# Optimization experiments

Measured on AMD Instinct MI355X. Metric: run time of the kernel, lower is better.

Reference implementation:

```python
import jax
import jax.numpy as jnp
from jax import lax
import numpy as np

N_LAYER = 8
SCALE = 4
H_CH = 128
Z_CH = 64


def conv2d(x, w, b=None, stride=1, pad=0):
    # x: NCHW, w: OIHW
    out = lax.conv_general_dilated(
        x, w, (stride, stride), [(pad, pad), (pad, pad)],
        dimension_numbers=("NCHW", "OIHW", "NCHW"))
    if b is not None:
        out = out + b[None, :, None, None]
    return out


def conv_transpose2d(x, w, stride):
    # torch ConvTranspose2d semantics, weight shape (in, out, kH, kW), no bias
    return lax.conv_transpose(
        x, w, (stride, stride), "VALID",
        dimension_numbers=("NCHW", "IOHW", "NCHW"), transpose_kernel=True)


def lstm_cell(inp, hidden, cell, gw, gb, tw, tb):
    # inp = inp + transform(hidden); gates fused into one conv (order f,i,o,s)
    inp = inp + conv2d(hidden, tw, tb, pad=2)
    gates = conv2d(inp, gw, gb, pad=2)
    f, i, o, s = jnp.split(gates, 4, axis=1)
    cell = jax.nn.sigmoid(f) * cell + jax.nn.sigmoid(i) * jnp.tanh(s)
    hidden = jax.nn.sigmoid(o) * jnp.tanh(cell)
    return hidden, cell


def setup_inputs() -> dict:
    key = jax.random.key(0)
    ks = jax.random.split(key, 24)
    b, xc, H, W = 64, 3, 64, 64
    vd, rd = 7, 256
    hs, ws = H // SCALE, W // SCALE
    enc_in = vd + rd + xc + H_CH   # 394
    dec_in = vd + rd + Z_CH        # 327

    def w_init(k, shape):
        fan_in = int(np.prod(shape[1:]))
        return jax.random.normal(k, shape, jnp.float32) / np.sqrt(fan_in)

    inp = {
        "x": jax.random.normal(ks[0], (b, xc, H, W), jnp.float32),
        "v": jax.random.normal(ks[1], (b, vd), jnp.float32),
        "r": jax.random.normal(ks[2], (b, rd, hs, ws), jnp.float32),
        "eps": jax.random.normal(ks[3], (N_LAYER, b, Z_CH, hs, ws), jnp.float32),
        "read_w": w_init(ks[4], (xc, xc, SCALE, SCALE)),
        "write_w": w_init(ks[5], (H_CH, H_CH, SCALE, SCALE)),  # (in,out,kH,kW)
        "prior_w": w_init(ks[6], (2 * Z_CH, H_CH, 5, 5)),
        "prior_b": jnp.zeros((2 * Z_CH,), jnp.float32),
        "post_w": w_init(ks[7], (2 * Z_CH, H_CH, 5, 5)),
        "post_b": jnp.zeros((2 * Z_CH,), jnp.float32),
        "enc_gw": w_init(ks[8], (4 * H_CH, enc_in, 5, 5)),
        "enc_gb": jnp.zeros((4 * H_CH,), jnp.float32),
        "enc_tw": w_init(ks[9], (enc_in, H_CH, 5, 5)),
        "enc_tb": jnp.zeros((enc_in,), jnp.float32),
        "dec_gw": w_init(ks[10], (4 * H_CH, dec_in, 5, 5)),
        "dec_gb": jnp.zeros((4 * H_CH,), jnp.float32),
        "dec_tw": w_init(ks[11], (dec_in, H_CH, 5, 5)),
        "dec_tb": jnp.zeros((dec_in,), jnp.float32),
        "obs_w": w_init(ks[12], (xc, H_CH, 1, 1)),
        "obs_b": jnp.zeros((xc,), jnp.float32),
    }
    return inp


def reference(x, v, r, eps, read_w, write_w, prior_w, prior_b, post_w, post_b,
              enc_gw, enc_gb, enc_tw, enc_tb, dec_gw, dec_gb, dec_tw, dec_tb,
              obs_w, obs_b):
    b, _, H, W = x.shape
    hs, ws = H // SCALE, W // SCALE
    dt = x.dtype
    h_enc = jnp.zeros((b, H_CH, hs, ws), dt)
    c_enc = jnp.zeros((b, H_CH, hs, ws), dt)
    h_dec = jnp.zeros((b, H_CH, hs, ws), dt)
    c_dec = jnp.zeros((b, H_CH, hs, ws), dt)
    u = jnp.zeros((b, H_CH, H, W), dt)

    xr = conv2d(x, read_w, stride=SCALE)            # (b, xc, hs, ws)
    vb = jnp.broadcast_to(v[:, :, None, None], (b, v.shape[1], hs, ws))
    rb = r if r.shape[2] == hs else jnp.tile(r, (1, 1, hs, ws))

    kl_loss = jnp.zeros((), dt)
    for t in range(N_LAYER):
        p_mu, p_lv = jnp.split(conv2d(h_dec, prior_w, prior_b, pad=2), 2, axis=1)
        h_enc, c_enc = lstm_cell(
            jnp.concatenate([h_dec, xr, vb, rb], axis=1),
            h_enc, c_enc, enc_gw, enc_gb, enc_tw, enc_tb)
        q_mu, q_lv = jnp.split(conv2d(h_enc, post_w, post_b, pad=2), 2, axis=1)
        z = q_mu + jnp.exp(0.5 * q_lv) * eps[t]
        h_dec, c_dec = lstm_cell(
            jnp.concatenate([z, vb, rb], axis=1),
            h_dec, c_dec, dec_gw, dec_gb, dec_tw, dec_tb)
        u = u + conv_transpose2d(h_dec, write_w, SCALE)
        # KL(q||p) with var = exp(logvar); log(var1/var0) = p_lv - q_lv
        kl = 0.5 * (jnp.exp(q_lv - p_lv)
                    + (p_mu - q_mu) ** 2 * jnp.exp(-p_lv)
                    - 1.0 + (p_lv - q_lv))
        kl_loss = kl_loss + kl.sum(axis=(1, 2, 3)).mean()

    canvas = jax.nn.sigmoid(conv2d(u, obs_w, obs_b))
    return canvas, kl_loss
```

## Files before the change

### kernel.cpp

```cpp
#include <hip/hip_runtime.h>
#include <hip/hip_bf16.h>

using bf16 = __hip_bfloat16;
typedef __attribute__((ext_vector_type(8))) short short8;
typedef __attribute__((ext_vector_type(4))) float f32x4;
typedef __attribute__((ext_vector_type(8))) int i32x8;
typedef __attribute__((ext_vector_type(4))) int i32x4;
typedef __attribute__((ext_vector_type(2))) int i32x2;

#define DEVI __device__ __forceinline__

#define MTOT 16384
#define PADS 25600

DEVI float sigm_(float x){ return 1.f/(1.f+expf(-x)); }

DEVI float s2f(short v){
  unsigned u = ((unsigned)(unsigned short)v) << 16;
  return __builtin_bit_cast(float, u);
}

DEVI long pidx_(int m){
  int nb = m>>8, iy=(m>>4)&15, ix=m&15;
  return (long)(nb*20 + iy + 2)*20 + (ix + 2);
}

DEVI unsigned char f2fp8(float x){
  int p = __builtin_amdgcn_cvt_pk_fp8_f32(x, 0.f, 0, false);
  return (unsigned char)(p & 0xFF);
}
DEVI float fp82f(unsigned char v){
  return __builtin_amdgcn_cvt_f32_fp8((int)v, 0);
}

DEVI void async16(const void* g, void* l) {
  __builtin_amdgcn_global_load_lds(
      (__attribute__((address_space(1))) void*)(unsigned long long)g,
      (__attribute__((address_space(3))) void*)(unsigned int)(unsigned long long)l,
      16, 0, 0);
}

template<int N> DEVI void waitbar(){
  if constexpr (N==0)      asm volatile("s_waitcnt vmcnt(0)\ns_barrier" ::: "memory");
  else if constexpr (N==3) asm volatile("s_waitcnt vmcnt(3)\ns_barrier" ::: "memory");
  else                     asm volatile("s_waitcnt vmcnt(6)\ns_barrier" ::: "memory");
}

template<int CA, int NS>
DEVI void g8_core(const unsigned char* __restrict__ A8,
                  const unsigned char* __restrict__ Bt8,
                  int m0, int n0, unsigned char* AsB, unsigned char* BsB,
                  f32x4 (&acc)[4][4])
{
  constexpr int Kp8 = NS*128;
  const int tid = threadIdx.x;
  const int wv = tid>>6, ln = tid&63;

  const int rr = tid>>3;
  const int lc = (tid&7) ^ (rr&7);
  long paRC[4], pbR[4];
  #pragma unroll
  for (int i=0;i<4;i++){
    int m = m0 + rr + (i<<5);
    paRC[i] = (long)(((m>>8)*20 + ((m>>4)&15))*20 + (m&15)) * CA;
    pbR[i]  = (long)(n0 + rr + (i<<5))*Kp8 + lc*16;
  }

  int cc = lc*16, tp = 0, ks = 0;
  auto stage = [&](int d){
    const int shiftC = ((tp/5)*20 + (tp%5)) * CA;
    char* la = (char*)AsB + d*16384 + (wv<<10);
    char* lb = (char*)BsB + d*16384 + (wv<<10);
    #pragma unroll
    for (int i=0;i<4;i++) async16(A8 + paRC[i] + shiftC + cc, la + i*4096);
    #pragma unroll
    for (int i=0;i<4;i++) async16(Bt8 + pbR[i] + ks, lb + i*4096);
    cc += 128; if (cc >= CA){ cc -= CA; tp++; }
    ks += 128;
  };

  const int wm = wv>>1, wn = wv&1;
  const int rA0 = (wm<<6) + (ln&15);
  const int rB0 = (wn<<6) + (ln&15);
  const int xa = ln&7;
  const int q2 = (ln>>4)<<1;
  const int c0 = ((q2    ) ^ xa)<<4;
  const int c1 = ((q2 | 1) ^ xa)<<4;

  stage(0);
  for (int t=0; t<NS; ++t) {
    asm volatile("s_waitcnt vmcnt(0)\ns_barrier" ::: "memory");
    if (t+1 < NS) stage((t+1)&1);

    const char* as_ = (const char*)AsB + (t&1)*16384;
    const char* bs_ = (const char*)BsB + (t&1)*16384;
    i32x8 af[4], bfr[4];
    #pragma unroll
    for (int f=0; f<4; f++){
      const char* p = as_ + ((rA0 + (f<<4))<<7);
      ((i32x4*)&af[f])[0] = *(const i32x4*)(p + c0);
      ((i32x4*)&af[f])[1] = *(const i32x4*)(p + c1);
    }
    #pragma unroll
    for (int f=0; f<4; f++){
      const char* p = bs_ + ((rB0 + (f<<4))<<7);
      ((i32x4*)&bfr[f])[0] = *(const i32x4*)(p + c0);
      ((i32x4*)&bfr[f])[1] = *(const i32x4*)(p + c1);
    }
    __builtin_amdgcn_s_setprio(1);
    #pragma unroll
    for (int mf=0; mf<4; mf++)
      #pragma unroll
      for (int nf=0; nf<4; nf++)
        acc[mf][nf] = __builtin_amdgcn_mfma_scale_f32_16x16x128_f8f6f4(
            af[mf], bfr[nf], acc[mf][nf], 0, 0, 0, 127, 0, 122);
    __builtin_amdgcn_s_setprio(0);
  }
}

template<int CA, int NS>
__global__ __launch_bounds__(256)
void conv_g8(const unsigned char* __restrict__ A8,
             const unsigned char* __restrict__ Bt8,
             const float* __restrict__ bias, bf16* __restrict__ outB)
{
  __shared__ alignas(16) unsigned char As[2][16384];
  __shared__ alignas(16) unsigned char Bs[2][16384];
  const int m0 = blockIdx.x<<7, n0 = blockIdx.y<<7;
  f32x4 acc[4][4] = {};
  g8_core<CA,NS>(A8, Bt8, m0, n0, &As[0][0], &Bs[0][0], acc);

  const int tid = threadIdx.x;
  const int wv = tid>>6, ln = tid&63;
  const int mb = m0 + ((wv>>1)<<6);
  const int nb = n0 + ((wv&1)<<6);
  const int ml = (ln>>4)<<2;
  const int nl = ln&15;
  #pragma unroll
  for (int mf=0; mf<4; mf++)
    #pragma unroll
    for (int j=0; j<4; j++) {
      const int m = mb + (mf<<4) + ml + j;
      #pragma unroll
      for (int nf=0; nf<4; nf++) {
        const int n = nb + (nf<<4) + nl;
        outB[((long)m<<9) + n] = __float2bfloat16(acc[mf][nf][j] + bias[n]);
      }
    }
}

__global__ __launch_bounds__(256)
void conv_tp8(const unsigned char* __restrict__ h8Dec,
              const unsigned char* __restrict__ h8Enc,
              const unsigned char* __restrict__ Bt8DP,
              const unsigned char* __restrict__ Bt8EncT,
              const float* __restrict__ dec_tb, const float* __restrict__ prior_b,
              const float* __restrict__ enc_tb,
              float* __restrict__ PriorO,
              unsigned char* __restrict__ sDec8, const bf16* __restrict__ STdec,
              unsigned char* __restrict__ sEnc8, const bf16* __restrict__ STenc,
              const bf16* __restrict__ hDecB)
{
  __shared__ alignas(16) unsigned char As[2][16384];
  __shared__ alignas(16) unsigned char Bs[2][16384];
  const int z = blockIdx.z;
  const int m0 = blockIdx.x<<7, n0 = blockIdx.y<<7;
  f32x4 acc[4][4] = {};
  if (z == 0) g8_core<128,25>(h8Dec, Bt8DP,   m0, n0, &As[0][0], &Bs[0][0], acc);
  else        g8_core<128,25>(h8Enc, Bt8EncT, m0, n0, &As[0][0], &Bs[0][0], acc);

  const int tid = threadIdx.x;
  const int wv = tid>>6, ln = tid&63;
  const int mb = m0 + ((wv>>1)<<6);
  const int nb = n0 + ((wv&1)<<6);
  const int ml = (ln>>4)<<2;
  const int nl = ln&15;
  #pragma unroll
  for (int mf=0; mf<4; mf++)
    #pragma unroll
    for (int j=0; j<4; j++) {
      const int m = mb + (mf<<4) + ml + j;
      const long pI = pidx_(m);
      #pragma unroll
      for (int nf=0; nf<4; nf++) {
        const int n = nb + (nf<<4) + nl;
        const float v = acc[mf][nf][j];
        if (z == 0) {
          if (n < 352) {
            float b  = (n < 327) ? dec_tb[n] : 0.f;
            float st = __bfloat162float(STdec[(long)m*352 + n]);
            sDec8[pI*352 + n] = f2fp8(v + b + st);
          } else if (n >= 384) {
            PriorO[((long)m<<7) + (n-384)] = v + prior_b[n-384];
          }
        } else {
          if (n < 416) {
            float b  = (n < 394) ? enc_tb[n] : 0.f;
            float st = __bfloat162float(STenc[(long)m*416 + n]);
            float e  = (n < 128) ? __bfloat162float(hDecB[(pI<<7) + n]) : 0.f;
            sEnc8[pI*416 + n] = f2fp8(v + b + st + e);
          }
        }
      }
    }
}

template<int CA, int EPI>
DEVI void conv_body(const bf16* __restrict__ A, const bf16* __restrict__ Bt,
                    bf16* __restrict__ outB,
                    int s0, int s1, int m0, int n0,
                    bf16* AsBase, bf16* BsBase)
{
  constexpr int Kp = 25*CA;
  const int NS = s1 - s0;

  const int tid = threadIdx.x;
  const int wv = tid>>6, ln = tid&63;

  const int rA = tid>>2;
  const int qs = ((tid&3) ^ ((rA>>1)&3))<<3;
  const int mA0 = m0 + rA, mA1 = m0 + 128 + rA;
  const long paA0 = ((long)(((mA0>>8)*20 + ((mA0>>4)&15))*20 + (mA0&15)))*CA + qs;
  const long paA1 = ((long)(((mA1>>8)*20 + ((mA1>>4)&15))*20 + (mA1&15)))*CA + qs;
  const long pbB  = (long)(n0 + rA)*Kp + qs;

  int kk0 = s0*32;
  int c0 = kk0 % CA;
  int tap = kk0 / CA;
  int kh = tap/5, kw = tap%5;
  int ks = kk0;

  auto stage = [&](int d){
    const long sh = (long)(kh*20 + kw)*CA + c0;
    char* la = (char*)AsBase + d*16384 + (wv<<10);
    char* lb = (char*)BsBase + d*8192  + (wv<<10);
    async16(A + paA0 + sh, la);
    async16(A + paA1 + sh, la + 8192);
    async16(Bt + pbB + ks, lb);
    ks += 32;
    c0 += 32; if (c0==CA){ c0=0; if(++kw==5){kw=0; ++kh;} }
  };

  f32x4 acc[4][4] = {};
  const int wm = wv>>1, wn = wv&1;
  const int rowA = (wm<<6) + (ln&15);
  const int rowB = (wn<<6) + (ln&15);
  const int kqA = (((ln>>4) ^ ((rowA>>1)&3))<<4);
  const int kqB = (((ln>>4) ^ ((rowB>>1)&3))<<4);

  stage(0); stage(1);
  int bc = 0, bs = 2;
  for (int t=0; t<NS; ++t) {
    if (t+1 < NS) waitbar<3>();
    else          waitbar<0>();
    if (t+2 < NS) stage(bs);

    const char* as_ = (const char*)AsBase + bc*16384;
    const char* bs_ = (const char*)BsBase + bc*8192;
    short8 af[4], bfr[4];
    #pragma unroll
    for (int mf=0; mf<4; mf++)
      af[mf] = *(const short8*)(as_ + ((rowA + (mf<<4))<<6) + kqA);
    #pragma unroll
    for (int nf=0; nf<4; nf++)
      bfr[nf] = *(const short8*)(bs_ + ((rowB + (nf<<4))<<6) + kqB);
    __builtin_amdgcn_s_setprio(1);
    #pragma unroll
    for (int mf=0; mf<4; mf++)
      #pragma unroll
      for (int nf=0; nf<4; nf++)
        acc[mf][nf] = __builtin_amdgcn_mfma_f32_16x16x32_bf16(af[mf], bfr[nf], acc[mf][nf], 0,0,0);
    __builtin_amdgcn_s_setprio(0);
    bc = (bc==2)?0:bc+1; bs = (bs==2)?0:bs+1;
  }

  const int mb = m0 + (wm<<6);
  const int nb = n0 + (wn<<6);
  const int ml = (ln>>4)<<2;
  const int nl = ln&15;
  #pragma unroll
  for (int mf=0; mf<4; mf++)
    #pragma unroll
    for (int j=0; j<4; j++) {
      const int m = mb + (mf<<4) + ml + j;
      #pragma unroll
      for (int nf=0; nf<4; nf++) {
        const int n = nb + (nf<<4) + nl;
        outB[((long)m<<7) + n] = __float2bfloat16(acc[mf][nf][j]);
      }
    }
}

__global__ __launch_bounds__(512)
void conv_post(const bf16* __restrict__ hEnc, const bf16* __restrict__ BtPost,
               bf16* __restrict__ PP)
{
  __shared__ alignas(16) bf16 As[3][256*32];
  __shared__ alignas(16) bf16 Bs[3][128*32];
  const int z = blockIdx.z;
  conv_body<128,6>(hEnc, BtPost, PP + (long)z*MTOT*128,
                   z*25, z*25+25, blockIdx.x<<8, 0, &As[0][0], &Bs[0][0]);
}

__global__ void repack_w_k(const float* __restrict__ w, bf16* __restrict__ Bt,
                           int O, int I, int CA, long total)
{
  long e = (long)blockIdx.x*256 + threadIdx.x;
  if (e >= total) return;
  const int Kp = 25*CA;
  int o = (int)(e / Kp);
  int k = (int)(e % Kp);
  int blk = k / CA, c = k % CA;
  float v = 0.f;
  if (o < O && c < I) v = w[((long)o*I + c)*25 + blk];
  Bt[e] = __float2bfloat16(v);
}

__global__ void repack_w8_k(const float* __restrict__ w, unsigned char* __restrict__ Bt,
                            int O, int I, int CA, int Kp8, long total)
{
  long e = (long)blockIdx.x*256 + threadIdx.x;
  if (e >= total) return;
  int o = (int)(e / Kp8);
  int k = (int)(e % Kp8);
  float v = 0.f;
  if (k < 25*CA) {
    int blk = k / CA, c = k % CA;
    if (o < O && c < I) v = w[((long)o*I + c)*25 + blk] * 32.0f;
  }
  Bt[e] = f2fp8(v);
}

__global__ void wcomb_k(const float* __restrict__ ww, const float* __restrict__ ow,
                        float* __restrict__ Wc)
{
  int idx = blockIdx.x*256 + threadIdx.x;
  if (idx >= 128*48) return;
  int c = idx / 48, rst = idx % 48;
  int pix = rst / 3, o = rst % 3;
  int ki = pix >> 2, kj = pix & 3;
  float a = 0.f;
  for (int mm=0; mm<128; mm++)
    a += ww[(((long)c*128 + mm)*4 + ki)*4 + kj] * ow[o*128 + mm];
  Wc[idx] = a;
}

__global__ void xr_k(const float* __restrict__ x, const float* __restrict__ rw,
                     float* __restrict__ xr)
{
  int idx = blockIdx.x*256 + threadIdx.x;
  if (idx >= MTOT*3) return;
  int m = idx / 3, o = idx % 3;
  int nb = m>>8, iy=(m>>4)&15, ix=m&15;
  float a = 0.f;
  for (int c=0;c<3;c++)
    for (int kh=0;kh<4;kh++)
      for (int kw=0;kw<4;kw++)
        a += x[((long)(nb*3+c)*64 + (iy*4+kh))*64 + (ix*4+kw)] * rw[((o*3+c)*4+kh)*4+kw];
  xr[idx] = a;
}

__global__ void st_enc_k(const float* __restrict__ xr, const float* __restrict__ v,
                         const float* __restrict__ r, bf16* __restrict__ ST)
{
  long g = (long)blockIdx.x*256 + threadIdx.x;
  if (g >= (long)MTOT*266) return;
  int m = (int)(g / 266), ch = (int)(g % 266);
  int nb = m>>8, sp = m&255;
  float val;
  if (ch < 3)       val = xr[m*3 + ch];
  else if (ch < 10) val = v[nb*7 + ch - 3];
  else              val = r[((long)nb*256 + (ch-10))*256 + sp];
  ST[(long)m*416 + 128 + ch] = __float2bfloat16(val);
}

__global__ void st_dec_k(const float* __restrict__ v, const float* __restrict__ r,
                         bf16* __restrict__ ST)
{
  long g = (long)blockIdx.x*256 + threadIdx.x;
  if (g >= (long)MTOT*263) return;
  int m = (int)(g / 263), ch = (int)(g % 263);
  int nb = m>>8, sp = m&255;
  float val;
  if (ch < 7) val = v[nb*7 + ch];
  else        val = r[((long)nb*256 + (ch-7))*256 + sp];
  ST[(long)m*352 + 64 + ch] = __float2bfloat16(val);
}

DEVI void lstm8_(const bf16* __restrict__ gates, float* __restrict__ cbuf,
                 bf16* __restrict__ hpad, unsigned char* __restrict__ h8,
                 int m, int c0, float* hout)
{
  long gb = ((long)m<<9) + c0;
  short8 gf = *(const short8*)(gates + gb);
  short8 gi = *(const short8*)(gates + gb + 128);
  short8 go = *(const short8*)(gates + gb + 256);
  short8 gs = *(const short8*)(gates + gb + 384);
  float* cb = cbuf + ((long)m<<7) + c0;
  f32x4 cv0 = *(f32x4*)cb;
  f32x4 cv1 = *(f32x4*)(cb+4);
  short8 hh;
  #pragma unroll
  for (int j=0;j<8;j++){
    float f = s2f(gf[j]);
    float i = s2f(gi[j]);
    float o = s2f(go[j]);
    float s = s2f(gs[j]);
    float cell = sigm_(f)*((j<4)?cv0[j]:cv1[j-4]) + sigm_(i)*tanhf(s);
    if (j<4) cv0[j]=cell; else cv1[j-4]=cell;
    float h = sigm_(o)*tanhf(cell);
    hout[j] = h;
    bf16 hb = __float2bfloat16(h);
    hh[j] = __builtin_bit_cast(short, hb);
  }
  *(f32x4*)cb = cv0;
  *(f32x4*)(cb+4) = cv1;
  long hp = (pidx_(m)<<7) + c0;
  *(short8*)(hpad + hp) = hh;
  int w0 = __builtin_amdgcn_cvt_pk_fp8_f32(hout[0], hout[1], 0, false);
  w0 = __builtin_amdgcn_cvt_pk_fp8_f32(hout[2], hout[3], w0, true);
  int w1 = __builtin_amdgcn_cvt_pk_fp8_f32(hout[4], hout[5], 0, false);
  w1 = __builtin_amdgcn_cvt_pk_fp8_f32(hout[6], hout[7], w1, true);
  i32x2 pw; pw[0]=w0; pw[1]=w1;
  *(i32x2*)(h8 + hp) = pw;
}

__global__ __launch_bounds__(256)
void lstm_k(const bf16* __restrict__ gates, float* __restrict__ cbuf,
            bf16* __restrict__ hpad, unsigned char* __restrict__ h8)
{
  const int tid = threadIdx.x;
  const int m = (blockIdx.x<<4) + (tid>>4);
  const int c0 = (tid&15)<<3;
  float h[8];
  lstm8_(gates, cbuf, hpad, h8, m, c0, h);
}

__global__ __launch_bounds__(256)
void lstm_wrc_k(const bf16* __restrict__ gates, float* __restrict__ cbuf,
                bf16* __restrict__ hpad, unsigned char* __restrict__ h8,
                const float* __restrict__ Wc, float* __restrict__ uc)
{
  __shared__ float Wl[6144];
  __shared__ float hl[16*128];
  const int tid = threadIdx.x;
  for (int i = tid; i < 6144; i += 256) Wl[i] = Wc[i];
  const int mloc = tid>>4;
  const int m = (blockIdx.x<<4) + mloc;
  const int c0 = (tid&15)<<3;
  float h[8];
  lstm8_(gates, cbuf, hpad, h8, m, c0, h);
  #pragma unroll
  for (int j=0;j<8;j++) hl[(mloc<<7) + c0 + j] = h[j];
  __syncthreads();

  const int pix = tid&15;
  const float* hrow = hl + (mloc<<7);
  float a0=0.f, a1=0.f, a2=0.f;
  #pragma unroll 4
  for (int c=0;c<128;c++) {
    float hv = hrow[c];
    const float* wl = Wl + c*48 + pix*3;
    a0 += hv*wl[0]; a1 += hv*wl[1]; a2 += hv*wl[2];
  }
  const int nb = m>>8, iy=(m>>4)&15, ix=m&15;
  const int ki = pix>>2, kj = pix&3;
  long ob = ((long)((nb<<6) + (iy<<2) + ki)*64 + (ix<<2) + kj)*3;
  uc[ob+0] += a0; uc[ob+1] += a1; uc[ob+2] += a2;
}

__global__ void zkl4_k(const bf16* __restrict__ PP, const float* __restrict__ pb,
                       const float* __restrict__ prior, const float* __restrict__ eps_t,
                       unsigned char* __restrict__ sDec8, float* __restrict__ part)
{
  __shared__ float wsum[4];
  const long PL = (long)MTOT*128;
  int idx = blockIdx.x*256 + threadIdx.x;
  int m = idx >> 6, c = idx & 63;
  float qm = pb[c], ql = pb[64 + c];
  #pragma unroll
  for (int z=0; z<4; ++z) {
    qm += __bfloat162float(PP[z*PL + ((long)m<<7) + c]);
    ql += __bfloat162float(PP[z*PL + ((long)m<<7) + 64 + c]);
  }
  long pbx = (long)m << 7;
  float pm = prior[pbx + c], pl = prior[pbx + 64 + c];
  int nb = m>>8, sp = m&255;
  float e = eps_t[((long)nb*64 + c)*256 + sp];
  float z = qm + expf(0.5f*ql)*e;
  long so = pidx_(m)*352 + c;
  sDec8[so] = f2fp8(fp82f(sDec8[so]) + z);
  float kl = expf(ql - pl) + (pm-qm)*(pm-qm)*expf(-pl) - 1.f + (pl - ql);
  #pragma unroll
  for (int off=32; off>0; off>>=1) kl += __shfl_down(kl, off);
  if ((threadIdx.x & 63) == 0) wsum[threadIdx.x >> 6] = kl;
  __syncthreads();
  if (threadIdx.x == 0)
    part[blockIdx.x] = wsum[0] + wsum[1] + wsum[2] + wsum[3];
}

__global__ void canvas_k(const float* __restrict__ uc, const float* __restrict__ ob,
                         float* __restrict__ out)
{
  int idx = blockIdx.x*256 + threadIdx.x;
  int x = idx & 63, y = (idx>>6)&63;
  int rem = idx >> 12;
  int o = rem % 3, n = rem / 3;
  float v = uc[((long)((n<<6)+y)*64 + x)*3 + o] + ob[o];
  out[idx] = 1.f/(1.f+expf(-v));
}

__global__ void klred_k(const float* __restrict__ part, float* __restrict__ out)
{
  __shared__ float wsum[4];
  float a = 0.f;
  for (int i = threadIdx.x; i < 32768; i += 256) a += part[i];
  #pragma unroll
  for (int off=32; off>0; off>>=1) a += __shfl_down(a, off);
  if ((threadIdx.x & 63) == 0) wsum[threadIdx.x >> 6] = a;
  __syncthreads();
  if (threadIdx.x == 0)
    out[786432] = (wsum[0] + wsum[1] + wsum[2] + wsum[3]) * (0.5f/64.f);
}

static const long O_BT_POST  = 0;
static const long O_BT_ENCT  = O_BT_POST  + 819200;
static const long O_BT_DP    = O_BT_ENCT  + 3276800;
static const long O_BT_ENCG  = O_BT_DP    + 3276800;
static const long O_BT_DECG  = O_BT_ENCG  + 10649600;
static const long O_WCOMB    = O_BT_DECG  + 9011200;
static const long O_XR       = O_WCOMB    + 24576;
static const long O_KLP      = O_XR       + 196608;
static const long O_STENC    = O_KLP      + 131072;
static const long O_STDEC    = O_STENC    + 13631488;
static const long O_HENC     = O_STDEC    + 11534336;
static const long O_HDEC     = O_HENC     + 6553600;
static const long O_SENC     = O_HDEC     + 6553600;
static const long O_SDEC     = O_SENC     + 21299200;
static const long O_CENC     = O_SDEC     + 18022400;
static const long O_CDEC     = O_CENC     + 8388608;
static const long O_PRIOR    = O_CDEC     + 8388608;
static const long O_H8E      = O_PRIOR    + 8388608;
static const long O_H8D      = O_H8E      + 3276800;
static const long O_PG       = O_H8D      + 3276800;
static const long O_UC       = O_PG       + 33554432;
static const long WS_TOTAL   = O_UC       + 3145728;

extern "C" void kernel_launch(void* const* d_in, const int* in_sizes, int n_in,
                              void* d_out, int out_size, void* d_ws, size_t ws_size,
                              hipStream_t stream)
{
  const float* x       = (const float*)d_in[0];
  const float* v       = (const float*)d_in[1];
  const float* r       = (const float*)d_in[2];
  const float* eps     = (const float*)d_in[3];
  const float* read_w  = (const float*)d_in[4];
  const float* write_w = (const float*)d_in[5];
  const float* prior_w = (const float*)d_in[6];
  const float* prior_b = (const float*)d_in[7];
  const float* post_w  = (const float*)d_in[8];
  const float* post_b  = (const float*)d_in[9];
  const float* enc_gw  = (const float*)d_in[10];
  const float* enc_gb  = (const float*)d_in[11];
  const float* enc_tw  = (const float*)d_in[12];
  const float* enc_tb  = (const float*)d_in[13];
  const float* dec_gw  = (const float*)d_in[14];
  const float* dec_gb  = (const float*)d_in[15];
  const float* dec_tw  = (const float*)d_in[16];
  const float* dec_tb  = (const float*)d_in[17];
  const float* obs_w   = (const float*)d_in[18];
  const float* obs_b   = (const float*)d_in[19];

  char* ws = (char*)d_ws;
  bf16* BtPost  = (bf16*)(ws + O_BT_POST);
  unsigned char* Bt8EncT = (unsigned char*)(ws + O_BT_ENCT);
  unsigned char* Bt8DP   = (unsigned char*)(ws + O_BT_DP);
  unsigned char* Bt8EncG = (unsigned char*)(ws + O_BT_ENCG);
  unsigned char* Bt8DecG = (unsigned char*)(ws + O_BT_DECG);
  float* Wcomb  = (float*)(ws + O_WCOMB);
  float* XR     = (float*)(ws + O_XR);
  float* KLpart = (float*)(ws + O_KLP);
  bf16* STenc   = (bf16*)(ws + O_STENC);
  bf16* STdec   = (bf16*)(ws + O_STDEC);
  bf16* hEnc    = (bf16*)(ws + O_HENC);
  bf16* hDec    = (bf16*)(ws + O_HDEC);
  unsigned char* sEnc8 = (unsigned char*)(ws + O_SENC);
  unsigned char* sDec8 = (unsigned char*)(ws + O_SDEC);
  float* cEnc   = (float*)(ws + O_CENC);
  float* cDec   = (float*)(ws + O_CDEC);
  float* PriorO = (float*)(ws + O_PRIOR);
  unsigned char* h8Enc = (unsigned char*)(ws + O_H8E);
  unsigned char* h8Dec = (unsigned char*)(ws + O_H8D);
  bf16* Gates   = (bf16*)(ws + O_PG);
  bf16* PostP   = (bf16*)(ws + O_PG + 16777216);
  float* Ucomb  = (float*)(ws + O_UC);
  float* out    = (float*)d_out;

  size_t clr = (size_t)WS_TOTAL; if (clr > ws_size) clr = ws_size;
  hipMemsetAsync(d_ws, 0, clr, stream);

  repack_w_k<<<1600, 256, 0, stream>>>(post_w, BtPost, 128, 128, 128, 128L*3200);
  repack_w8_k<<<6400, 256, 0, stream>>>(enc_tw, Bt8EncT, 394, 128, 128, 3200, 512L*3200);
  repack_w8_k<<<4800, 256, 0, stream>>>(dec_tw, Bt8DP, 327, 128, 128, 3200, 384L*3200);
  repack_w8_k<<<1600, 256, 0, stream>>>(prior_w, Bt8DP + 384L*3200, 128, 128, 128, 3200, 128L*3200);
  repack_w8_k<<<20992, 256, 0, stream>>>(enc_gw, Bt8EncG, 512, 394, 416, 82*128, 512L*10496);
  repack_w8_k<<<17664, 256, 0, stream>>>(dec_gw, Bt8DecG, 512, 327, 352, 69*128, 512L*8832);
  wcomb_k<<<24, 256, 0, stream>>>(write_w, obs_w, Wcomb);
  xr_k<<<192, 256, 0, stream>>>(x, read_w, XR);
  st_enc_k<<<(int)(((long)MTOT*266 + 255)/256), 256, 0, stream>>>(XR, v, r, STenc);
  st_dec_k<<<(int)(((long)MTOT*263 + 255)/256), 256, 0, stream>>>(v, r, STdec);

  for (int t = 0; t < 8; ++t) {
    conv_tp8<<<dim3(128,4,2), 256, 0, stream>>>(
        h8Dec, h8Enc, Bt8DP, Bt8EncT, dec_tb, prior_b, enc_tb,
        PriorO, sDec8, STdec, sEnc8, STenc, hDec);
    conv_g8<416,82><<<dim3(128,4), 256, 0, stream>>>(sEnc8, Bt8EncG, enc_gb, Gates);
    lstm_k<<<1024, 256, 0, stream>>>(Gates, cEnc, hEnc, h8Enc);
    conv_post<<<dim3(64,1,4), 512, 0, stream>>>(hEnc, BtPost, PostP);
    zkl4_k<<<4096, 256, 0, stream>>>(PostP, post_b, PriorO,
                                     eps + (long)t*64*64*256, sDec8,
                                     KLpart + (long)t*4096);
    conv_g8<352,69><<<dim3(128,4), 256, 0, stream>>>(sDec8, Bt8DecG, dec_gb, Gates);
    lstm_wrc_k<<<1024, 256, 0, stream>>>(Gates, cDec, hDec, h8Dec, Wcomb, Ucomb);
  }

  canvas_k<<<3072, 256, 0, stream>>>(Ucomb, obs_b, out);
  klred_k<<<1, 256, 0, stream>>>(KLpart, out);
}
```

Measured before the change: 2.620 ms.

## Move posterior conv to FP8 MFMA and vectorize GEMM epilogues through LDS

The posterior convolution moves from a bf16 MFMA kernel to the shared FP8 g8_core path, reading the fp8 encoder hidden state with a split-K over four tap ranges. All FP8 conv kernels now stage accumulators through LDS in a transposed epilogue so each thread writes 32 contiguous outputs with vector stores and packed fp8 conversions, replacing scattered scalar stores. Padded bias arrays remove per-element branches in the epilogue. This cuts store and epilogue overhead and the cost of the post conv, at the price of lower precision in the posterior mu/logvar and extra LDS round trips.

```diff
diff --git a/kernel.cpp b/kernel.cpp
--- a/kernel.cpp
+++ b/kernel.cpp
@@ -19,6 +19,10 @@
   unsigned u = ((unsigned)(unsigned short)v) << 16;
   return __builtin_bit_cast(float, u);
 }
+DEVI short f2s(float x){
+  bf16 hb = __float2bfloat16(x);
+  return __builtin_bit_cast(short, hb);
+}
 
 DEVI long pidx_(int m){
   int nb = m>>8, iy=(m>>4)&15, ix=m&15;
@@ -40,19 +44,13 @@
       16, 0, 0);
 }
 
-template<int N> DEVI void waitbar(){
-  if constexpr (N==0)      asm volatile("s_waitcnt vmcnt(0)\ns_barrier" ::: "memory");
-  else if constexpr (N==3) asm volatile("s_waitcnt vmcnt(3)\ns_barrier" ::: "memory");
-  else                     asm volatile("s_waitcnt vmcnt(6)\ns_barrier" ::: "memory");
-}
-
-template<int CA, int NS>
+template<int CA, int NSF>
 DEVI void g8_core(const unsigned char* __restrict__ A8,
                   const unsigned char* __restrict__ Bt8,
                   int m0, int n0, unsigned char* AsB, unsigned char* BsB,
-                  f32x4 (&acc)[4][4])
-{
-  constexpr int Kp8 = NS*128;
+                  f32x4 (&acc)[4][4], int ns0, int nst)
+{
+  constexpr int Kp8 = NSF*128;
   const int tid = threadIdx.x;
   const int wv = tid>>6, ln = tid&63;
 
@@ -66,7 +64,7 @@
     pbR[i]  = (long)(n0 + rr + (i<<5))*Kp8 + lc*16;
   }
 
-  int cc = lc*16, tp = 0, ks = 0;
+  int cc = lc*16, tp = ns0, ks = ns0*128;
   auto stage = [&](int d){
     const int shiftC = ((tp/5)*20 + (tp%5)) * CA;
     char* la = (char*)AsB + d*16384 + (wv<<10);
@@ -88,9 +86,9 @@
   const int c1 = ((q2 | 1) ^ xa)<<4;
 
   stage(0);
-  for (int t=0; t<NS; ++t) {
+  for (int t=0; t<nst; ++t) {
     asm volatile("s_waitcnt vmcnt(0)\ns_barrier" ::: "memory");
-    if (t+1 < NS) stage((t+1)&1);
+    if (t+1 < nst) stage((t+1)&1);
 
     const char* as_ = (const char*)AsB + (t&1)*16384;
     const char* bs_ = (const char*)BsB + (t&1)*16384;
@@ -118,35 +116,84 @@
   }
 }
 
+template<typename F>
+DEVI void tepi(f32x4 (&acc)[4][4], float* fl, F&& emit)
+{
+  const int tid = threadIdx.x;
+  const int wv = tid>>6, ln = tid&63;
+  const int wm = wv>>1, wn = wv&1;
+  const int ml = (ln>>4)<<2, nl = ln&15;
+  for (int h=0; h<2; ++h) {
+    __syncthreads();
+    if (wm == h) {
+      #pragma unroll
+      for (int mf=0; mf<4; mf++)
+        #pragma unroll
+        for (int j=0; j<4; j++) {
+          const int r = (mf<<4) + ml + j;
+          #pragma unroll
+          for (int nf=0; nf<4; nf++)
+            fl[r*132 + (wn<<6) + (nf<<4) + nl] = acc[mf][nf][j];
+        }
+    }
+    __syncthreads();
+    {
+      const int r = tid>>2, cb = (tid&3)<<5;
+      float v[32];
+      #pragma unroll
+      for (int k=0; k<8; k++)
+        *(f32x4*)(v + (k<<2)) = *(const f32x4*)(fl + r*132 + cb + (k<<2));
+      emit(h, r, cb, v);
+    }
+  }
+}
+
 template<int CA, int NS>
 __global__ __launch_bounds__(256)
 void conv_g8(const unsigned char* __restrict__ A8,
              const unsigned char* __restrict__ Bt8,
              const float* __restrict__ bias, bf16* __restrict__ outB)
 {
-  __shared__ alignas(16) unsigned char As[2][16384];
-  __shared__ alignas(16) unsigned char Bs[2][16384];
+  __shared__ alignas(16) unsigned char SMEM[65536];
   const int m0 = blockIdx.x<<7, n0 = blockIdx.y<<7;
   f32x4 acc[4][4] = {};
-  g8_core<CA,NS>(A8, Bt8, m0, n0, &As[0][0], &Bs[0][0], acc);
-
-  const int tid = threadIdx.x;
-  const int wv = tid>>6, ln = tid&63;
-  const int mb = m0 + ((wv>>1)<<6);
-  const int nb = n0 + ((wv&1)<<6);
-  const int ml = (ln>>4)<<2;
-  const int nl = ln&15;
-  #pragma unroll
-  for (int mf=0; mf<4; mf++)
-    #pragma unroll
-    for (int j=0; j<4; j++) {
-      const int m = mb + (mf<<4) + ml + j;
+  g8_core<CA,NS>(A8, Bt8, m0, n0, SMEM, SMEM+32768, acc, 0, NS);
+
+  tepi(acc, (float*)SMEM, [&](int h, int r, int cb, float* v){
+    const long m = m0 + (h<<6) + r;
+    const int n = n0 + cb;
+    short8 o[4];
+    #pragma unroll
+    for (int k=0; k<4; k++){
+      f32x4 b0 = *(const f32x4*)(bias + n + (k<<3));
+      f32x4 b1 = *(const f32x4*)(bias + n + (k<<3) + 4);
       #pragma unroll
-      for (int nf=0; nf<4; nf++) {
-        const int n = nb + (nf<<4) + nl;
-        outB[((long)m<<9) + n] = __float2bfloat16(acc[mf][nf][j] + bias[n]);
-      }
+      for (int i=0; i<4; i++) o[k][i]   = f2s(v[(k<<3)+i]   + b0[i]);
+      #pragma unroll
+      for (int i=0; i<4; i++) o[k][4+i] = f2s(v[(k<<3)+4+i] + b1[i]);
     }
+    bf16* dst = outB + (m<<9) + n;
+    #pragma unroll
+    for (int k=0; k<4; k++) *(short8*)(dst + (k<<3)) = o[k];
+  });
+}
+
+DEVI void store32fp8(unsigned char* dst, const float* f){
+  i32x4 w0, w1;
+  #pragma unroll
+  for (int p=0; p<4; p++){
+    int d = __builtin_amdgcn_cvt_pk_fp8_f32(f[4*p],   f[4*p+1], 0, false);
+    d     = __builtin_amdgcn_cvt_pk_fp8_f32(f[4*p+2], f[4*p+3], d, true);
+    w0[p] = d;
+  }
+  #pragma unroll
+  for (int p=0; p<4; p++){
+    int d = __builtin_amdgcn_cvt_pk_fp8_f32(f[16+4*p],   f[16+4*p+1], 0, false);
+    d     = __builtin_amdgcn_cvt_pk_fp8_f32(f[16+4*p+2], f[16+4*p+3], d, true);
+    w1[p] = d;
+  }
+  *(i32x4*)dst        = w0;
+  *(i32x4*)(dst + 16) = w1;
 }
 
 __global__ __launch_bounds__(256)
@@ -154,166 +201,94 @@
               const unsigned char* __restrict__ h8Enc,
               const unsigned char* __restrict__ Bt8DP,
               const unsigned char* __restrict__ Bt8EncT,
-              const float* __restrict__ dec_tb, const float* __restrict__ prior_b,
-              const float* __restrict__ enc_tb,
+              const float* __restrict__ tbDec352, const float* __restrict__ prior_b,
+              const float* __restrict__ tbEnc416,
               float* __restrict__ PriorO,
               unsigned char* __restrict__ sDec8, const bf16* __restrict__ STdec,
               unsigned char* __restrict__ sEnc8, const bf16* __restrict__ STenc,
               const bf16* __restrict__ hDecB)
 {
-  __shared__ alignas(16) unsigned char As[2][16384];
-  __shared__ alignas(16) unsigned char Bs[2][16384];
+  __shared__ alignas(16) unsigned char SMEM[65536];
   const int z = blockIdx.z;
   const int m0 = blockIdx.x<<7, n0 = blockIdx.y<<7;
   f32x4 acc[4][4] = {};
-  if (z == 0) g8_core<128,25>(h8Dec, Bt8DP,   m0, n0, &As[0][0], &Bs[0][0], acc);
-  else        g8_core<128,25>(h8Enc, Bt8EncT, m0, n0, &As[0][0], &Bs[0][0], acc);
-
-  const int tid = threadIdx.x;
-  const int wv = tid>>6, ln = tid&63;
-  const int mb = m0 + ((wv>>1)<<6);
-  const int nb = n0 + ((wv&1)<<6);
-  const int ml = (ln>>4)<<2;
-  const int nl = ln&15;
-  #pragma unroll
-  for (int mf=0; mf<4; mf++)
-    #pragma unroll
-    for (int j=0; j<4; j++) {
-      const int m = mb + (mf<<4) + ml + j;
-      const long pI = pidx_(m);
-      #pragma unroll
-      for (int nf=0; nf<4; nf++) {
-        const int n = nb + (nf<<4) + nl;
-        const float v = acc[mf][nf][j];
-        if (z == 0) {
-          if (n < 352) {
-            float b  = (n < 327) ? dec_tb[n] : 0.f;
-            float st = __bfloat162float(STdec[(long)m*352 + n]);
-            sDec8[pI*352 + n] = f2fp8(v + b + st);
-          } else if (n >= 384) {
-            PriorO[((long)m<<7) + (n-384)] = v + prior_b[n-384];
-          }
-        } else {
-          if (n < 416) {
-            float b  = (n < 394) ? enc_tb[n] : 0.f;
-            float st = __bfloat162float(STenc[(long)m*416 + n]);
-            float e  = (n < 128) ? __bfloat162float(hDecB[(pI<<7) + n]) : 0.f;
-            sEnc8[pI*416 + n] = f2fp8(v + b + st + e);
+  if (z == 0) g8_core<128,25>(h8Dec, Bt8DP,   m0, n0, SMEM, SMEM+32768, acc, 0, 25);
+  else        g8_core<128,25>(h8Enc, Bt8EncT, m0, n0, SMEM, SMEM+32768, acc, 0, 25);
+
+  tepi(acc, (float*)SMEM, [&](int h, int r, int cb, float* v){
+    const long m = m0 + (h<<6) + r;
+    const int n = n0 + cb;
+    if (z == 0) {
+      if (n0 == 384) {
+        float* dst = PriorO + (m<<7) + cb;
+        #pragma unroll
+        for (int k=0; k<8; k++){
+          f32x4 b = *(const f32x4*)(prior_b + cb + (k<<2));
+          f32x4 x = *(const f32x4*)(v + (k<<2));
+          *(f32x4*)(dst + (k<<2)) = x + b;
+        }
+      } else if (n < 352) {
+        const long pI = pidx_(m);
+        float f[32];
+        #pragma unroll
+        for (int k=0; k<4; k++){
+          short8 st = *(const short8*)(STdec + m*352 + n + (k<<3));
+          #pragma unroll
+          for (int i=0; i<8; i++)
+            f[(k<<3)+i] = v[(k<<3)+i] + tbDec352[n+(k<<3)+i] + s2f(st[i]);
+        }
+        store32fp8(sDec8 + pI*352 + n, f);
+      }
+    } else {
+      if (n < 416) {
+        const long pI = pidx_(m);
+        float f[32];
+        #pragma unroll
+        for (int k=0; k<4; k++){
+          short8 st = *(const short8*)(STenc + m*416 + n + (k<<3));
+          #pragma unroll
+          for (int i=0; i<8; i++)
+            f[(k<<3)+i] = v[(k<<3)+i] + tbEnc416[n+(k<<3)+i] + s2f(st[i]);
+        }
+        if (n0 == 0) {
+          #pragma unroll
+          for (int k=0; k<4; k++){
+            short8 e = *(const short8*)(hDecB + (pI<<7) + cb + (k<<3));
+            #pragma unroll
+            for (int i=0; i<8; i++) f[(k<<3)+i] += s2f(e[i]);
           }
         }
+        store32fp8(sEnc8 + pI*416 + n, f);
       }
     }
-}
-
-template<int CA, int EPI>
-DEVI void conv_body(const bf16* __restrict__ A, const bf16* __restrict__ Bt,
-                    bf16* __restrict__ outB,
-                    int s0, int s1, int m0, int n0,
-                    bf16* AsBase, bf16* BsBase)
-{
-  constexpr int Kp = 25*CA;
-  const int NS = s1 - s0;
-
-  const int tid = threadIdx.x;
-  const int wv = tid>>6, ln = tid&63;
-
-  const int rA = tid>>2;
-  const int qs = ((tid&3) ^ ((rA>>1)&3))<<3;
-  const int mA0 = m0 + rA, mA1 = m0 + 128 + rA;
-  const long paA0 = ((long)(((mA0>>8)*20 + ((mA0>>4)&15))*20 + (mA0&15)))*CA + qs;
-  const long paA1 = ((long)(((mA1>>8)*20 + ((mA1>>4)&15))*20 + (mA1&15)))*CA + qs;
-  const long pbB  = (long)(n0 + rA)*Kp + qs;
-
-  int kk0 = s0*32;
-  int c0 = kk0 % CA;
-  int tap = kk0 / CA;
-  int kh = tap/5, kw = tap%5;
-  int ks = kk0;
-
-  auto stage = [&](int d){
-    const long sh = (long)(kh*20 + kw)*CA + c0;
-    char* la = (char*)AsBase + d*16384 + (wv<<10);
-    char* lb = (char*)BsBase + d*8192  + (wv<<10);
-    async16(A + paA0 + sh, la);
-    async16(A + paA1 + sh, la + 8192);
-    async16(Bt + pbB + ks, lb);
-    ks += 32;
-    c0 += 32; if (c0==CA){ c0=0; if(++kw==5){kw=0; ++kh;} }
-  };
-
+  });
+}
+
+__global__ __launch_bounds__(256)
+void conv_p8(const unsigned char* __restrict__ h8Enc,
+             const unsigned char* __restrict__ Bt8Post,
+             bf16* __restrict__ PP)
+{
+  __shared__ alignas(16) unsigned char SMEM[65536];
+  const int z = blockIdx.z;
+  const int s0[4]  = {0, 7, 13, 19};
+  const int len[4] = {7, 6, 6, 6};
+  const int m0 = blockIdx.x<<7;
   f32x4 acc[4][4] = {};
-  const int wm = wv>>1, wn = wv&1;
-  const int rowA = (wm<<6) + (ln&15);
-  const int rowB = (wn<<6) + (ln&15);
-  const int kqA = (((ln>>4) ^ ((rowA>>1)&3))<<4);
-  const int kqB = (((ln>>4) ^ ((rowB>>1)&3))<<4);
-
-  stage(0); stage(1);
-  int bc = 0, bs = 2;
-  for (int t=0; t<NS; ++t) {
-    if (t+1 < NS) waitbar<3>();
-    else          waitbar<0>();
-    if (t+2 < NS) stage(bs);
-
-    const char* as_ = (const char*)AsBase + bc*16384;
-    const char* bs_ = (const char*)BsBase + bc*8192;
-    short8 af[4], bfr[4];
-    #pragma unroll
-    for (int mf=0; mf<4; mf++)
-      af[mf] = *(const short8*)(as_ + ((rowA + (mf<<4))<<6) + kqA);
-    #pragma unroll
-    for (int nf=0; nf<4; nf++)
-      bfr[nf] = *(const short8*)(bs_ + ((rowB + (nf<<4))<<6) + kqB);
-    __builtin_amdgcn_s_setprio(1);
-    #pragma unroll
-    for (int mf=0; mf<4; mf++)
+  g8_core<128,25>(h8Enc, Bt8Post, m0, 0, SMEM, SMEM+32768, acc, s0[z], len[z]);
+
+  bf16* plane = PP + (long)z*MTOT*128;
+  tepi(acc, (float*)SMEM, [&](int h, int r, int cb, float* v){
+    const long m = m0 + (h<<6) + r;
+    bf16* dst = plane + (m<<7) + cb;
+    short8 o[4];
+    #pragma unroll
+    for (int k=0; k<4; k++)
       #pragma unroll
-      for (int nf=0; nf<4; nf++)
-        acc[mf][nf] = __builtin_amdgcn_mfma_f32_16x16x32_bf16(af[mf], bfr[nf], acc[mf][nf], 0,0,0);
-    __builtin_amdgcn_s_setprio(0);
-    bc = (bc==2)?0:bc+1; bs = (bs==2)?0:bs+1;
-  }
-
-  const int mb = m0 + (wm<<6);
-  const int nb = n0 + (wn<<6);
-  const int ml = (ln>>4)<<2;
-  const int nl = ln&15;
-  #pragma unroll
-  for (int mf=0; mf<4; mf++)
-    #pragma unroll
-    for (int j=0; j<4; j++) {
-      const int m = mb + (mf<<4) + ml + j;
-      #pragma unroll
-      for (int nf=0; nf<4; nf++) {
-        const int n = nb + (nf<<4) + nl;
-        outB[((long)m<<7) + n] = __float2bfloat16(acc[mf][nf][j]);
-      }
-    }
-}
-
-__global__ __launch_bounds__(512)
-void conv_post(const bf16* __restrict__ hEnc, const bf16* __restrict__ BtPost,
-               bf16* __restrict__ PP)
-{
-  __shared__ alignas(16) bf16 As[3][256*32];
-  __shared__ alignas(16) bf16 Bs[3][128*32];
-  const int z = blockIdx.z;
-  conv_body<128,6>(hEnc, BtPost, PP + (long)z*MTOT*128,
-                   z*25, z*25+25, blockIdx.x<<8, 0, &As[0][0], &Bs[0][0]);
-}
-
-__global__ void repack_w_k(const float* __restrict__ w, bf16* __restrict__ Bt,
-                           int O, int I, int CA, long total)
-{
-  long e = (long)blockIdx.x*256 + threadIdx.x;
-  if (e >= total) return;
-  const int Kp = 25*CA;
-  int o = (int)(e / Kp);
-  int k = (int)(e % Kp);
-  int blk = k / CA, c = k % CA;
-  float v = 0.f;
-  if (o < O && c < I) v = w[((long)o*I + c)*25 + blk];
-  Bt[e] = __float2bfloat16(v);
+      for (int i=0; i<8; i++) o[k][i] = f2s(v[(k<<3)+i]);
+    #pragma unroll
+    for (int k=0; k<4; k++) *(short8*)(dst + (k<<3)) = o[k];
+  });
 }
 
 __global__ void repack_w8_k(const float* __restrict__ w, unsigned char* __restrict__ Bt,
@@ -329,6 +304,14 @@
     if (o < O && c < I) v = w[((long)o*I + c)*25 + blk] * 32.0f;
   }
   Bt[e] = f2fp8(v);
+}
+
+__global__ void padbias_k(const float* __restrict__ etb, const float* __restrict__ dtb,
+                          float* __restrict__ tbe, float* __restrict__ tbd)
+{
+  int i = threadIdx.x;
+  if (i < 416) tbe[i] = (i < 394) ? etb[i] : 0.f;
+  if (i < 352) tbd[i] = (i < 327) ? dtb[i] : 0.f;
 }
 
 __global__ void wcomb_k(const float* __restrict__ ww, const float* __restrict__ ow,
@@ -410,8 +393,7 @@
     if (j<4) cv0[j]=cell; else cv1[j-4]=cell;
     float h = sigm_(o)*tanhf(cell);
     hout[j] = h;
-    bf16 hb = __float2bfloat16(h);
-    hh[j] = __builtin_bit_cast(short, hb);
+    hh[j] = f2s(h);
   }
   *(f32x4*)cb = cv0;
   *(f32x4*)(cb+4) = cv1;
@@ -544,7 +526,9 @@
 static const long O_H8D      = O_H8E      + 3276800;
 static const long O_PG       = O_H8D      + 3276800;
 static const long O_UC       = O_PG       + 33554432;
-static const long WS_TOTAL   = O_UC       + 3145728;
+static const long O_TBE      = O_UC       + 3145728;
+static const long O_TBD      = O_TBE      + 2048;
+static const long WS_TOTAL   = O_TBD      + 2048;
 
 extern "C" void kernel_launch(void* const* d_in, const int* in_sizes, int n_in,
                               void* d_out, int out_size, void* d_ws, size_t ws_size,
@@ -572,7 +556,7 @@
   const float* obs_b   = (const float*)d_in[19];
 
   char* ws = (char*)d_ws;
-  bf16* BtPost  = (bf16*)(ws + O_BT_POST);
+  unsigned char* Bt8Post = (unsigned char*)(ws + O_BT_POST);
   unsigned char* Bt8EncT = (unsigned char*)(ws + O_BT_ENCT);
   unsigned char* Bt8DP   = (unsigned char*)(ws + O_BT_DP);
   unsigned char* Bt8EncG = (unsigned char*)(ws + O_BT_ENCG);
@@ -594,17 +578,20 @@
   bf16* Gates   = (bf16*)(ws + O_PG);
   bf16* PostP   = (bf16*)(ws + O_PG + 16777216);
   float* Ucomb  = (float*)(ws + O_UC);
+  float* TBE    = (float*)(ws + O_TBE);
+  float* TBD    = (float*)(ws + O_TBD);
   float* out    = (float*)d_out;
 
   size_t clr = (size_t)WS_TOTAL; if (clr > ws_size) clr = ws_size;
   hipMemsetAsync(d_ws, 0, clr, stream);
 
-  repack_w_k<<<1600, 256, 0, stream>>>(post_w, BtPost, 128, 128, 128, 128L*3200);
+  repack_w8_k<<<1600, 256, 0, stream>>>(post_w, Bt8Post, 128, 128, 128, 3200, 128L*3200);
   repack_w8_k<<<6400, 256, 0, stream>>>(enc_tw, Bt8EncT, 394, 128, 128, 3200, 512L*3200);
   repack_w8_k<<<4800, 256, 0, stream>>>(dec_tw, Bt8DP, 327, 128, 128, 3200, 384L*3200);
   repack_w8_k<<<1600, 256, 0, stream>>>(prior_w, Bt8DP + 384L*3200, 128, 128, 128, 3200, 128L*3200);
   repack_w8_k<<<20992, 256, 0, stream>>>(enc_gw, Bt8EncG, 512, 394, 416, 82*128, 512L*10496);
   repack_w8_k<<<17664, 256, 0, stream>>>(dec_gw, Bt8DecG, 512, 327, 352, 69*128, 512L*8832);
+  padbias_k<<<1, 512, 0, stream>>>(enc_tb, dec_tb, TBE, TBD);
   wcomb_k<<<24, 256, 0, stream>>>(write_w, obs_w, Wcomb);
   xr_k<<<192, 256, 0, stream>>>(x, read_w, XR);
   st_enc_k<<<(int)(((long)MTOT*266 + 255)/256), 256, 0, stream>>>(XR, v, r, STenc);
@@ -612,11 +599,11 @@
 
   for (int t = 0; t < 8; ++t) {
     conv_tp8<<<dim3(128,4,2), 256, 0, stream>>>(
-        h8Dec, h8Enc, Bt8DP, Bt8EncT, dec_tb, prior_b, enc_tb,
+        h8Dec, h8Enc, Bt8DP, Bt8EncT, TBD, prior_b, TBE,
         PriorO, sDec8, STdec, sEnc8, STenc, hDec);
     conv_g8<416,82><<<dim3(128,4), 256, 0, stream>>>(sEnc8, Bt8EncG, enc_gb, Gates);
     lstm_k<<<1024, 256, 0, stream>>>(Gates, cEnc, hEnc, h8Enc);
-    conv_post<<<dim3(64,1,4), 512, 0, stream>>>(hEnc, BtPost, PostP);
+    conv_p8<<<dim3(128,1,4), 256, 0, stream>>>(h8Enc, Bt8Post, PostP);
     zkl4_k<<<4096, 256, 0, stream>>>(PostP, post_b, PriorO,
                                      eps + (long)t*64*64*256, sDec8,
                                      KLpart + (long)t*4096);
```

Measured after the change: 2.715 ms. 3.6% more time.
